# Kernel optimization log

Measured on AMD Instinct MI355X. Metric: run time of the kernel, lower is better.

Reference implementation:

```python
import jax, jax.numpy as jnp
import numpy as np


def setup_inputs() -> dict:
    key = jax.random.key(0)
    ks = jax.random.split(key, 7)
    T, B, X, H = 256, 64, 512, 2048
    s_ih = 1.0 / np.sqrt(H)
    return {
        "input": jax.random.normal(ks[0], (T, B, X), dtype=jnp.float32),
        "h_0": jax.random.normal(ks[1], (B, H), dtype=jnp.float32),
        "c_0": jax.random.normal(ks[2], (B, H), dtype=jnp.float32),
        "w_ih": jax.random.normal(ks[3], (4 * H, X), dtype=jnp.float32) * s_ih,
        "w_hh": jax.random.normal(ks[4], (4 * H, H), dtype=jnp.float32) * s_ih,
        "b_ih": jax.random.normal(ks[5], (4 * H,), dtype=jnp.float32) * s_ih,
        "b_hh": jax.random.normal(ks[6], (4 * H,), dtype=jnp.float32) * s_ih,
    }


def reference(input, h_0, c_0, w_ih, w_hh, b_ih, b_hh):
    H = h_0.shape[-1]
    # Precompute input projections for all timesteps in one big GEMM: [T,B,4H]
    x_proj = jnp.einsum("tbx,gx->tbg", input, w_ih) + b_ih + b_hh

    def step(carry, xg):
        h, c = carry
        gates = xg + h @ w_hh.T  # [B, 4H]
        i, f, g, o = jnp.split(gates, 4, axis=-1)  # torch LSTMCell gate order
        i = jax.nn.sigmoid(i)
        f = jax.nn.sigmoid(f)
        g = jnp.tanh(g)
        o = jax.nn.sigmoid(o)
        c_new = f * c + i * g
        h_new = o * jnp.tanh(c_new)
        y = jax.nn.softmax(h_new, axis=-1)  # per-step softmax over hidden dim
        return (h_new, c_new), y

    (h_T, c_T), ys = jax.lax.scan(step, (h_0, c_0), x_proj)
    return ys, h_T, c_T
```

## Files before the change

### kernel.cpp

```cpp
#include <hip/hip_runtime.h>

#define Tn 256
#define Bn 64
#define Xn 512
#define Hn 2048
#define Gn 8192
#define NWG 256

typedef short bf16x8 __attribute__((ext_vector_type(8)));
typedef float f32x4 __attribute__((ext_vector_type(4)));
typedef unsigned uint32x4 __attribute__((ext_vector_type(4)));

#define AL(p)    __hip_atomic_load((p), __ATOMIC_RELAXED, __HIP_MEMORY_SCOPE_AGENT)
#define AS(p, v) __hip_atomic_store((p), (v), __ATOMIC_RELAXED, __HIP_MEMORY_SCOPE_AGENT)
#define AADD(p, v) __hip_atomic_fetch_add((p), (v), __ATOMIC_RELAXED, __HIP_MEMORY_SCOPE_AGENT)

static __device__ __forceinline__ unsigned short f2bf(float f) {
    unsigned int u = __builtin_bit_cast(unsigned int, f);
    u += 0x7fffu + ((u >> 16) & 1u);
    return (unsigned short)(u >> 16);
}
static __device__ __forceinline__ float bf2f(unsigned short s) {
    unsigned int u = ((unsigned int)s) << 16;
    return __builtin_bit_cast(float, u);
}
static __device__ __forceinline__ void cvt4(const float* __restrict__ s,
                                            unsigned short* __restrict__ d, int i) {
    float4 v = ((const float4*)s)[i];
    ushort4 o;
    o.x = f2bf(v.x); o.y = f2bf(v.y); o.z = f2bf(v.z); o.w = f2bf(v.w);
    ((ushort4*)d)[i] = o;
}
static __device__ __forceinline__ float sigm(float x) {
    return 1.f / (1.f + __expf(-x));
}
static __device__ __forceinline__ float ftanh(float x) {
    float e = __expf(2.f * x);
    return (e - 1.f) / (e + 1.f);
}

template <int RING>
static __device__ __forceinline__ size_t hoff(int t) {
    if constexpr (RING) return (size_t)((t * 97) % 257) * 262144;
    else                return (size_t)(t & 1) * 262144;
}
template <int RING>
static __device__ __forceinline__ bf16x8 ldh(const unsigned short* p) {
    if constexpr (RING) {
        return *(const bf16x8*)p;
    } else {
        unsigned* q = (unsigned*)p;
        uint32x4 v;
        v[0] = AL(q + 0); v[1] = AL(q + 1); v[2] = AL(q + 2); v[3] = AL(q + 3);
        return __builtin_bit_cast(bf16x8, v);
    }
}
template <int RING>
static __device__ __forceinline__ float ldh1(const unsigned short* hb, int idx) {
    if constexpr (RING) {
        return bf2f(hb[idx]);
    } else {
        unsigned d = AL((unsigned*)(hb + (idx & ~1)));
        return bf2f((idx & 1) ? (unsigned short)(d >> 16) : (unsigned short)(d & 0xffffu));
    }
}

static __device__ __forceinline__ void oct_wait(const unsigned* sh, int base,
                                                unsigned target, int l) {
    if (!target) return;
    const unsigned* p = sh + (base + (l & 7)) * 16;
    for (;;) {
        unsigned a = (l < 8) ? AL(p) : target;
        if (__all(a >= target)) break;
        __builtin_amdgcn_s_sleep(1);
    }
}
static __device__ __forceinline__ void half_wait(const unsigned* hf, unsigned target, int l) {
    if (!target) return;
    const unsigned* p = hf + (l & 31) * 16;
    for (;;) {
        unsigned a = (l < 32) ? AL(p) : target;
        if (__all(a >= target)) break;
        __builtin_amdgcn_s_sleep(1);
    }
}

template <int RING>
static __device__ __forceinline__ void solo_softmax(const unsigned short* hb, int row,
                                                    float* __restrict__ yr, int l) {
    float v[32];
    float m = -1e30f;
    #pragma unroll
    for (int i = 0; i < 32; ++i) {
        int idx = (i * 8 + (l >> 3)) * 512 + row * 8 + (l & 7);
        v[i] = ldh1<RING>(hb, idx);
        m = fmaxf(m, v[i]);
    }
    #pragma unroll
    for (int off = 32; off; off >>= 1) m = fmaxf(m, __shfl_xor(m, off));
    float s = 0.f;
    #pragma unroll
    for (int i = 0; i < 32; ++i) { v[i] = __expf(v[i] - m); s += v[i]; }
    #pragma unroll
    for (int off = 32; off; off >>= 1) s += __shfl_xor(s, off);
    float inv = 1.f / s;
    #pragma unroll
    for (int i = 0; i < 32; ++i) yr[i * 64 + l] = v[i] * inv;
}

__global__ void prologue3(const float* __restrict__ x, const float* __restrict__ h0,
                          const float* __restrict__ b_ih, const float* __restrict__ b_hh,
                          const float* __restrict__ w_ih,
                          unsigned short* __restrict__ Xb, unsigned short* __restrict__ XFrag,
                          unsigned short* __restrict__ hb0, float* __restrict__ bias,
                          unsigned* __restrict__ flags)
{
    int i = blockIdx.x * blockDim.x + threadIdx.x;
    const int n_x  = Tn * Bn * Xn / 4;
    const int n_xf = Gn * Xn / 4;
    const int n_h  = Bn * Hn / 4;
    const int n_b  = Gn / 4;
    if (i < n_x) { cvt4(x, Xb, i); return; }
    i -= n_x;
    if (i < n_xf) {
        int wg = i >> 12, r = i & 4095;
        int c = r >> 7, k = (r & 127) * 4;
        int g = c >> 3, u = c & 7;
        float4 v = *(const float4*)(w_ih + (size_t)(g * Hn + wg * 8 + u) * Xn + k);
        ushort4 o;
        o.x = f2bf(v.x); o.y = f2bf(v.y); o.z = f2bf(v.z); o.w = f2bf(v.w);
        int ct = c >> 4, kk = k >> 5, l = ((k >> 3) & 3) * 16 + (c & 15);
        *(ushort4*)((char*)XFrag + (size_t)wg * 32768 + (size_t)((ct * 16 + kk) * 64 + l) * 16 + (k & 7) * 2) = o;
        return;
    }
    i -= n_xf;
    if (i < n_h) {
        int flat = i * 4;
        int row = flat >> 11, unit0 = flat & 2047;
        float4 v = ((const float4*)h0)[i];
        ushort4 o;
        o.x = f2bf(v.x); o.y = f2bf(v.y); o.z = f2bf(v.z); o.w = f2bf(v.w);
        int dst = (((unit0 >> 3) << 6) + row) * 8 + (unit0 & 7);
        *(ushort4*)(hb0 + dst) = o;
        return;
    }
    i -= n_h;
    if (i < n_b) {
        float4 a = ((const float4*)b_ih)[i];
        float4 b = ((const float4*)b_hh)[i];
        ((float4*)bias)[i] = make_float4(a.x + b.x, a.y + b.y, a.z + b.z, a.w + b.w);
        return;
    }
    i -= n_b;
    if (i < 1024) flags[i] = 0u;
}

#define MFMA4(a0v, a1v) \
    acc00 = __builtin_amdgcn_mfma_f32_16x16x32_bf16((a0v), b0, acc00, 0, 0, 0); \
    acc10 = __builtin_amdgcn_mfma_f32_16x16x32_bf16((a1v), b0, acc10, 0, 0, 0); \
    acc01 = __builtin_amdgcn_mfma_f32_16x16x32_bf16((a0v), b1, acc01, 0, 0, 0); \
    acc11 = __builtin_amdgcn_mfma_f32_16x16x32_bf16((a1v), b1, acc11, 0, 0, 0);

template <int RING>
__global__ __launch_bounds__(512, 1) void lstm_persist9(
    const unsigned short* __restrict__ Xb, const unsigned short* __restrict__ XFrag,
    const float* __restrict__ bias, const float* __restrict__ c0,
    char* __restrict__ hbase, const float* __restrict__ w_hh,
    float* __restrict__ ys, float* __restrict__ hT, float* __restrict__ cT,
    unsigned* __restrict__ flags)
{
    extern __shared__ char smem[];
    const unsigned short* LW = (const unsigned short*)smem;
    float* RED = (float*)(smem + 131072);

    const int wg  = blockIdx.x;
    const int tid = threadIdx.x;
    const int U0  = wg * 8;

    for (int i = tid; i < 32 * 512; i += 512) {
        int c = i >> 9, k = (i & 511) * 4;
        int g = c >> 3, u = c & 7;
        float4 v = *(const float4*)(w_hh + (size_t)(g * Hn + U0 + u) * Hn + k);
        ushort4 o;
        o.x = f2bf(v.x); o.y = f2bf(v.y); o.z = f2bf(v.z); o.w = f2bf(v.w);
        int ct = c >> 4, kk = k >> 5, l = ((k >> 3) & 3) * 16 + (c & 15);
        *(ushort4*)(smem + ((size_t)((ct * 64 + kk) * 64 + l) * 16 + (k & 7) * 2)) = o;
    }
    __syncthreads();

    const int w = tid >> 6, l = tid & 63;
    const int lm = l & 15, lh = l >> 4;
    const int kh = w >> 1, rblk = w & 1, rb = rblk * 32;
    const int kk0 = kh * 16;
    const int kx0 = kh * 4;

    const int u  = lm & 7;
    const bool hi = (lm & 8) != 0;

    float bi = 0.f, bf_ = 0.f, bg = 0.f, bo = 0.f;
    float cs[2][2] = {{0.f, 0.f}, {0.f, 0.f}};
    if (kh == 0) {
        bi  = bias[0 * Hn + U0 + u];
        bf_ = bias[1 * Hn + U0 + u];
        bg  = bias[2 * Hn + U0 + u];
        bo  = bias[3 * Hn + U0 + u];
        #pragma unroll
        for (int s = 0; s < 2; ++s)
            #pragma unroll
            for (int j = 0; j < 2; ++j)
                cs[s][j] = c0[(size_t)(rb + s * 16 + 4 * lh + (hi ? 2 : 0) + j) * Hn + U0 + u];
    }

    const char* xfb = (const char*)XFrag + (size_t)wg * 32768;
    const unsigned* gate_f = flags + rblk * 512;

    for (int t = 0; t < Tn; ++t) {
        const unsigned short* hb = (const unsigned short*)(hbase + hoff<RING>(t));
        unsigned short* hn = (unsigned short*)(hbase + hoff<RING>(t + 1));

        f32x4 acc00 = {0,0,0,0}, acc01 = {0,0,0,0}, acc10 = {0,0,0,0}, acc11 = {0,0,0,0};

        {
            const unsigned short* xa0 = Xb + (size_t)(t * 64 + rb + lm) * Xn + lh * 8;
            const unsigned short* xa1 = xa0 + 16 * Xn;
            bf16x8 xA0[4], xA1[4];
            #pragma unroll
            for (int j = 0; j < 4; ++j) {
                xA0[j] = *(const bf16x8*)(xa0 + (kx0 + j) * 32);
                xA1[j] = *(const bf16x8*)(xa1 + (kx0 + j) * 32);
            }
            #pragma unroll
            for (int kkl = 0; kkl < 4; ++kkl) {
                bf16x8 b0 = *(const bf16x8*)(xfb + ((size_t)((0 * 16 + kx0 + kkl) * 64 + l) << 4));
                bf16x8 b1 = *(const bf16x8*)(xfb + ((size_t)((1 * 16 + kx0 + kkl) * 64 + l) << 4));
                MFMA4(xA0[kkl], xA1[kkl]);
            }
        }

        oct_wait(gate_f, kh * 8, (unsigned)t * 8u, l);

        {
            const unsigned short* ha0 = hb + (size_t)(rb + lm) * 8;
            const unsigned short* ha1 = ha0 + 128;
            bf16x8 aP0[4], aP1[4];
            #pragma unroll
            for (int j = 0; j < 4; ++j) {
                int g = (kk0 + j) * 4 + lh;
                aP0[j] = ldh<RING>(ha0 + (size_t)g * 512);
                aP1[j] = ldh<RING>(ha1 + (size_t)g * 512);
            }
            #pragma unroll 4
            for (int kkl = 0; kkl < 16; ++kkl) {
                bf16x8 a0v = aP0[kkl & 3], a1v = aP1[kkl & 3];
                if (kkl < 12) {
                    int g = (kk0 + kkl + 4) * 4 + lh;
                    aP0[kkl & 3] = ldh<RING>(ha0 + (size_t)g * 512);
                    aP1[kkl & 3] = ldh<RING>(ha1 + (size_t)g * 512);
                }
                bf16x8 b0 = *(const bf16x8*)(LW + ((size_t)((0 * 64 + kk0 + kkl) * 64 + l) << 3));
                bf16x8 b1 = *(const bf16x8*)(LW + ((size_t)((1 * 64 + kk0 + kkl) * 64 + l) << 3));
                MFMA4(a0v, a1v);
            }
        }

        if (kh != 0) {
            int slot = (kh - 1) * 2 + rblk;
            int base = (slot * 64 + l) * 4;
            *(f32x4*)(RED + 0 * 1536 + base) = acc00;
            *(f32x4*)(RED + 1 * 1536 + base) = acc01;
            *(f32x4*)(RED + 2 * 1536 + base) = acc10;
            *(f32x4*)(RED + 3 * 1536 + base) = acc11;
        }
        __syncthreads();

        if (kh == 0) {
            #pragma unroll
            for (int p = 0; p < 3; ++p) {
                int base = ((p * 2 + rblk) * 64 + l) * 4;
                acc00 += *(const f32x4*)(RED + 0 * 1536 + base);
                acc01 += *(const f32x4*)(RED + 1 * 1536 + base);
                acc10 += *(const f32x4*)(RED + 2 * 1536 + base);
                acc11 += *(const f32x4*)(RED + 3 * 1536 + base);
            }
            f32x4 sA[2], sB[2];
            #pragma unroll
            for (int r = 0; r < 4; ++r) {
                sA[0][r] = __shfl_xor(acc00[r], 8); sB[0][r] = __shfl_xor(acc01[r], 8);
                sA[1][r] = __shfl_xor(acc10[r], 8); sB[1][r] = __shfl_xor(acc11[r], 8);
            }
            #pragma unroll
            for (int s = 0; s < 2; ++s) {
                f32x4 aA = s ? acc10 : acc00;
                f32x4 aB = s ? acc11 : acc01;
                #pragma unroll
                for (int j = 0; j < 2; ++j) {
                    int r = (hi ? 2 : 0) + j;
                    float gi = (hi ? sA[s][r] : aA[r]) + bi;
                    float gf = (hi ? aA[r] : sA[s][r]) + bf_;
                    float gg = (hi ? sB[s][r] : aB[r]) + bg;
                    float go = (hi ? aB[r] : sB[s][r]) + bo;
                    float iv = sigm(gi), fv = sigm(gf), gv = ftanh(gg), ov = sigm(go);
                    float cc = cs[s][j];
                    float cn = fv * cc + iv * gv;
                    float hv = ov * ftanh(cn);
                    cs[s][j] = cn;
                    int rowg = rb + s * 16 + 4 * lh + (hi ? 2 : 0) + j;
                    unsigned short mybf = f2bf(hv);
                    unsigned other = (unsigned)__shfl_xor((int)(unsigned)mybf, 1);
                    if (!(u & 1)) {
                        AS((unsigned*)(hn + (size_t)wg * 512 + rowg * 8 + u),
                           (unsigned)mybf | (other << 16));
                    }
                    if (t == Tn - 1) {
                        size_t off = (size_t)rowg * Hn + U0 + u;
                        hT[off] = hv;
                        cT[off] = cn;
                    }
                }
            }
            asm volatile("s_waitcnt vmcnt(0)" ::: "memory");
            if (l == 0) AADD((unsigned*)(flags + rblk * 512 + (wg >> 3) * 16), 1u);
        }
        __syncthreads();

        if (w == 7 && t > 0) {
            int srow = wg - (t & 3) * 64;
            if (srow >= 0 && srow < Bn) {
                half_wait(flags + (srow >= 32 ? 512 : 0), (unsigned)t * 8u, l);
                solo_softmax<RING>(hb, srow, ys + ((size_t)(t - 1) * Bn + srow) * Hn, l);
            }
        }
    }

    if (w == 7 && wg < Bn) {
        const unsigned short* hfin = (const unsigned short*)(hbase + hoff<RING>(Tn));
        half_wait(flags + (wg >= 32 ? 512 : 0), (unsigned)Tn * 8u, l);
        solo_softmax<RING>(hfin, wg, ys + ((size_t)(Tn - 1) * Bn + wg) * Hn, l);
    }
}

extern "C" void kernel_launch(void* const* d_in, const int* in_sizes, int n_in,
                              void* d_out, int out_size, void* d_ws, size_t ws_size,
                              hipStream_t stream) {
    const float* input = (const float*)d_in[0];
    const float* h0    = (const float*)d_in[1];
    const float* c0    = (const float*)d_in[2];
    const float* w_ih  = (const float*)d_in[3];
    const float* w_hh  = (const float*)d_in[4];
    const float* b_ih  = (const float*)d_in[5];
    const float* b_hh  = (const float*)d_in[6];

    float* ys = (float*)d_out;
    float* hT = ys + (size_t)Tn * Bn * Hn;
    float* cT = hT + (size_t)Bn * Hn;

    char* wsb = (char*)d_ws;
    unsigned short* Xb  = (unsigned short*)wsb;
    unsigned short* XF  = (unsigned short*)(wsb + 16777216);
    float* bias         = (float*)(wsb + 25165824);
    unsigned* flags     = (unsigned*)(wsb + 25198592);
    char* hbase         = wsb + 25202688;
    const size_t need_ring = 25202688 + (size_t)257 * 262144;

    const int prol_items = Tn * Bn * Xn / 4 + Gn * Xn / 4 + Bn * Hn / 4 + Gn / 4 + 1024;
    const int prol_blocks = (prol_items + 255) / 256;
    prologue3<<<dim3(prol_blocks), dim3(256), 0, stream>>>(
        input, h0, b_ih, b_hh, w_ih, Xb, XF, (unsigned short*)hbase, bias, flags);

    if (ws_size >= need_ring) {
        (void)hipFuncSetAttribute((const void*)lstm_persist9<1>,
                                  hipFuncAttributeMaxDynamicSharedMemorySize, 155648);
        lstm_persist9<1><<<dim3(NWG), dim3(512), 155648, stream>>>(
            Xb, XF, bias, c0, hbase, w_hh, ys, hT, cT, flags);
    } else {
        (void)hipFuncSetAttribute((const void*)lstm_persist9<0>,
                                  hipFuncAttributeMaxDynamicSharedMemorySize, 155648);
        lstm_persist9<0><<<dim3(NWG), dim3(512), 155648, stream>>>(
            Xb, XF, bias, c0, hbase, w_hh, ys, hT, cT, flags);
    }
}
```

Baseline: 1.896 ms.

## Wait per h-shard flag and consume shards as they arrive in a staggered order

The recurrent GEMM used to wait for all eight producer-group flags of its K-slice before loading any h data. It now waits on one shard flag at a time, loads that shard's two K-chunks, and runs the MFMAs on the previous shard while the next one is fetched. Each workgroup starts at a different shard (wg & 7) so the polling traffic is spread out. This lets compute overlap with late producers, at the cost of more flag polling, since every lane now reads its flag, and a shorter prefetch depth.

```diff
diff --git a/kernel.cpp b/kernel.cpp
--- a/kernel.cpp
+++ b/kernel.cpp
@@ -65,12 +65,10 @@
     }
 }
 
-static __device__ __forceinline__ void oct_wait(const unsigned* sh, int base,
-                                                unsigned target, int l) {
+static __device__ __forceinline__ void shard_wait(const unsigned* p, unsigned target) {
     if (!target) return;
-    const unsigned* p = sh + (base + (l & 7)) * 16;
     for (;;) {
-        unsigned a = (l < 8) ? AL(p) : target;
+        unsigned a = AL(p);
         if (__all(a >= target)) break;
         __builtin_amdgcn_s_sleep(1);
     }
@@ -162,7 +160,7 @@
     acc11 = __builtin_amdgcn_mfma_f32_16x16x32_bf16((a1v), b1, acc11, 0, 0, 0);
 
 template <int RING>
-__global__ __launch_bounds__(512, 1) void lstm_persist9(
+__global__ __launch_bounds__(512, 1) void lstm_persist10(
     const unsigned short* __restrict__ Xb, const unsigned short* __restrict__ XFrag,
     const float* __restrict__ bias, const float* __restrict__ c0,
     char* __restrict__ hbase, const float* __restrict__ w_hh,
@@ -213,6 +211,7 @@
 
     const char* xfb = (const char*)XFrag + (size_t)wg * 32768;
     const unsigned* gate_f = flags + rblk * 512;
+    const int so0 = wg & 7;
 
     for (int t = 0; t < Tn; ++t) {
         const unsigned short* hb = (const unsigned short*)(hbase + hoff<RING>(t));
@@ -237,29 +236,41 @@
             }
         }
 
-        oct_wait(gate_f, kh * 8, (unsigned)t * 8u, l);
-
         {
             const unsigned short* ha0 = hb + (size_t)(rb + lm) * 8;
             const unsigned short* ha1 = ha0 + 128;
-            bf16x8 aP0[4], aP1[4];
-            #pragma unroll
-            for (int j = 0; j < 4; ++j) {
-                int g = (kk0 + j) * 4 + lh;
-                aP0[j] = ldh<RING>(ha0 + (size_t)g * 512);
-                aP1[j] = ldh<RING>(ha1 + (size_t)g * 512);
-            }
-            #pragma unroll 4
-            for (int kkl = 0; kkl < 16; ++kkl) {
-                bf16x8 a0v = aP0[kkl & 3], a1v = aP1[kkl & 3];
-                if (kkl < 12) {
-                    int g = (kk0 + kkl + 4) * 4 + lh;
-                    aP0[kkl & 3] = ldh<RING>(ha0 + (size_t)g * 512);
-                    aP1[kkl & 3] = ldh<RING>(ha1 + (size_t)g * 512);
+            const unsigned tgt = (unsigned)t * 8u;
+            bf16x8 pA0[2][2], pA1[2][2];
+
+            {
+                const int so = so0;
+                shard_wait(gate_f + (kh * 8 + so) * 16, tgt);
+                const int gA = (kk0 + 2 * so) * 4 + lh, gB = (kk0 + 2 * so + 1) * 4 + lh;
+                pA0[0][0] = ldh<RING>(ha0 + (size_t)gA * 512);
+                pA1[0][0] = ldh<RING>(ha1 + (size_t)gA * 512);
+                pA0[0][1] = ldh<RING>(ha0 + (size_t)gB * 512);
+                pA1[0][1] = ldh<RING>(ha1 + (size_t)gB * 512);
+            }
+            #pragma unroll
+            for (int s = 0; s < 8; ++s) {
+                const int cur = s & 1;
+                if (s < 7) {
+                    const int son = (so0 + s + 1) & 7;
+                    shard_wait(gate_f + (kh * 8 + son) * 16, tgt);
+                    const int gA = (kk0 + 2 * son) * 4 + lh, gB = (kk0 + 2 * son + 1) * 4 + lh;
+                    pA0[cur ^ 1][0] = ldh<RING>(ha0 + (size_t)gA * 512);
+                    pA1[cur ^ 1][0] = ldh<RING>(ha1 + (size_t)gA * 512);
+                    pA0[cur ^ 1][1] = ldh<RING>(ha0 + (size_t)gB * 512);
+                    pA1[cur ^ 1][1] = ldh<RING>(ha1 + (size_t)gB * 512);
                 }
-                bf16x8 b0 = *(const bf16x8*)(LW + ((size_t)((0 * 64 + kk0 + kkl) * 64 + l) << 3));
-                bf16x8 b1 = *(const bf16x8*)(LW + ((size_t)((1 * 64 + kk0 + kkl) * 64 + l) << 3));
-                MFMA4(a0v, a1v);
+                const int soc = (so0 + s) & 7;
+                #pragma unroll
+                for (int j = 0; j < 2; ++j) {
+                    const int kkl = 2 * soc + j;
+                    bf16x8 b0 = *(const bf16x8*)(LW + ((size_t)((0 * 64 + kk0 + kkl) * 64 + l) << 3));
+                    bf16x8 b1 = *(const bf16x8*)(LW + ((size_t)((1 * 64 + kk0 + kkl) * 64 + l) << 3));
+                    MFMA4(pA0[cur][j], pA1[cur][j]);
+                }
             }
         }
 
@@ -368,14 +379,14 @@
         input, h0, b_ih, b_hh, w_ih, Xb, XF, (unsigned short*)hbase, bias, flags);
 
     if (ws_size >= need_ring) {
-        (void)hipFuncSetAttribute((const void*)lstm_persist9<1>,
+        (void)hipFuncSetAttribute((const void*)lstm_persist10<1>,
                                   hipFuncAttributeMaxDynamicSharedMemorySize, 155648);
-        lstm_persist9<1><<<dim3(NWG), dim3(512), 155648, stream>>>(
+        lstm_persist10<1><<<dim3(NWG), dim3(512), 155648, stream>>>(
             Xb, XF, bias, c0, hbase, w_hh, ys, hT, cT, flags);
     } else {
-        (void)hipFuncSetAttribute((const void*)lstm_persist9<0>,
+        (void)hipFuncSetAttribute((const void*)lstm_persist10<0>,
                                   hipFuncAttributeMaxDynamicSharedMemorySize, 155648);
-        lstm_persist9<0><<<dim3(NWG), dim3(512), 155648, stream>>>(
+        lstm_persist10<0><<<dim3(NWG), dim3(512), 155648, stream>>>(
             Xb, XF, bias, c0, hbase, w_hh, ys, hT, cT, flags);
     }
 }
```

Result: slower. 2.093 ms (+10.4%).
